# Optimization experiments

Measured on AMD Instinct MI355X. Metric: run time of the kernel, lower is better.

The kernel has to match this reference:

```python
import jax, jax.numpy as jnp
import numpy as np
import math

NUM_HEADS = 16  # power of two -> simple ALiBi slope formula

def alibi_slopes(num_heads: int) -> jnp.ndarray:
    # num_heads is a power of two here; general formula per Press et al. 2022
    k = 1 << (num_heads.bit_length() - 1)
    ratio = 2.0 ** (-8.0 / k)
    slopes = ratio ** np.arange(1, 1 + k)
    if num_heads != k:
        ratio2 = 2.0 ** (-8.0 / (2 * k))
        rest = (ratio2 ** np.arange(1, 1 + 2 * k, 2))[: num_heads - k]
        slopes = np.concatenate([slopes, rest])
    return jnp.asarray(slopes, dtype=jnp.float32).reshape(1, -1, 1, 1)


def setup_inputs() -> dict:
    key = jax.random.key(0)
    kq, kk, kv, km = jax.random.split(key, 4)
    B, H, S, D = 1, NUM_HEADS, 2048, 64
    query = jax.random.normal(kq, (B, H, S, D), dtype=jnp.float32)
    k_ = jax.random.normal(kk, (B, H, S, D), dtype=jnp.float32)
    value = jax.random.normal(kv, (B, H, S, D), dtype=jnp.float32)
    # padding-style boolean mask [B, S]; keep position 0 always valid
    mask = jax.random.randint(km, (B, S), 0, 2).astype(bool)
    mask = mask.at[:, 0].set(True)
    return {"query": query, "key": k_, "value": value, "mask": mask}


def reference(query, key, value, mask):
    B, H, S, D = query.shape
    scale = 1.0 / math.sqrt(D)
    # scores: [B, H, Sq, Sk]
    scores = jnp.einsum("bhqd,bhkd->bhqk", query, key) * scale
    # causal ALiBi bias: distances arange(1-S, 1) -> shape (1, H, 1, S)
    distances = jnp.arange(1 - S, 1, dtype=jnp.float32)
    bias = distances[None, None, None, :] * alibi_slopes(H)
    scores = scores + bias
    # boolean padding mask [B, S] -> [B, 1, 1, S]
    blocked = jnp.finfo(scores.dtype).min
    scores = jnp.where(mask[:, None, None, :], scores, blocked)
    weights = jax.nn.softmax(scores, axis=-1)
    # dropout_prob = 0.0 (eval) -> identity
    return jnp.einsum("bhqk,bhkd->bhqd", weights, value)
```

## Files before the change

kernel.cpp:

```cpp
#include <hip/hip_runtime.h>


constexpr int   S_LEN  = 2048;
constexpr int   D_DIM  = 64;
constexpr int   H_NUM  = 16;
constexpr int   QT     = 128;
constexpr int   K_TILE = 64;
constexpr int   NTILE  = S_LEN / K_TILE;
constexpr int   MAXNC  = 8;
constexpr int   QB     = S_LEN / QT;
constexpr int   PROWSTR= 36;
constexpr float SCL    = 0.18033688f;
constexpr float L2E    = 1.44269504f;
constexpr float MASKED = -50000.0f;
constexpr float CUTOFF = 40.0f;

typedef short bf16x8 __attribute__((ext_vector_type(8)));
typedef short bf16x4 __attribute__((ext_vector_type(4)));
typedef float f32x4  __attribute__((ext_vector_type(4)));

__device__ inline short f2bf(float f) {
    union { float f; unsigned u; } x; x.f = f;
    return (short)((x.u + 0x7fffu + ((x.u >> 16) & 1u)) >> 16);
}

__device__ inline unsigned pack2bf(float a, float b) {
#if __has_builtin(__builtin_amdgcn_cvt_pk_bf16_f32)
    auto p = __builtin_amdgcn_cvt_pk_bf16_f32(a, b);
    unsigned u; __builtin_memcpy(&u, &p, 4); return u;
#else
    return (unsigned)(unsigned short)f2bf(a) | ((unsigned)(unsigned short)f2bf(b) << 16);
#endif
}

__device__ inline float fexp2(float x) {
#if __has_builtin(__builtin_amdgcn_exp2f)
    return __builtin_amdgcn_exp2f(x);
#else
    return exp2f(x);
#endif
}

__device__ inline unsigned permb(unsigned hi, unsigned lo, unsigned sel) {
#if __has_builtin(__builtin_amdgcn_perm)
    return __builtin_amdgcn_perm(hi, lo, sel);
#else
    return (sel == 0x05040100u) ? ((lo & 0xffffu) | (hi << 16))
                                : ((lo >> 16) | (hi & 0xffff0000u));
#endif
}

__device__ inline void load_lds16(const void* g, void* l) {
    __builtin_amdgcn_global_load_lds((const __attribute__((address_space(1))) void*)g,
                                     (__attribute__((address_space(3))) void*)l, 16, 0, 0);
}

__device__ inline int head_t0(int h) {
    const float slope_l2e = exp2f(-0.5f * (float)(h + 1)) * L2E;
    const float kmin = 2047.0f - CUTOFF / slope_l2e;
    return kmin <= 0.0f ? 0 : ((int)kmin) >> 6;
}
__device__ inline int head_nc(int h) {
    const int nt = NTILE - head_t0(h);
    const int nc = (nt + 3) >> 2;
    return nc > MAXNC ? MAXNC : nc;
}

__global__ __launch_bounds__(256)
void preprocess_kernel(const float* __restrict__ Km, const float* __restrict__ Vm,
                       const void* __restrict__ maskp,
                       short* __restrict__ Kswz, short* __restrict__ Vswz,
                       float* __restrict__ Bias)
{
    __shared__ int mask_is_i32;
    const int tid = threadIdx.x;
    const int kt = blockIdx.x, h = blockIdx.y;
    if (kt < head_t0(h)) return;

    const int kbase = kt * K_TILE;
    const size_t tbase = ((size_t)h * S_LEN + kbase) * D_DIM;
    short* Kd = Kswz + ((size_t)h * NTILE + kt) * 4096;
    short* Vd = Vswz + ((size_t)h * NTILE + kt) * 4096;

    if (tid < 64) {
        const unsigned v = ((const unsigned*)maskp)[tid];
        const unsigned long long b = __ballot(v <= 1u);
        if (tid == 0) mask_is_i32 = (b == ~0ULL);
    }

    #pragma unroll
    for (int it = 0; it < 2; ++it) {
        const int idx = it * 256 + tid;
        const int key = idx >> 3, c = idx & 7;
        const float* src = Km + tbase + key * 64 + c * 8;
        float4 a = *(const float4*)src;
        float4 b = *(const float4*)(src + 4);
        unsigned u[4] = { pack2bf(a.x, a.y), pack2bf(a.z, a.w),
                          pack2bf(b.x, b.y), pack2bf(b.z, b.w) };
        bf16x8 kp; __builtin_memcpy(&kp, u, 16);
        *(bf16x8*)(Kd + key * 64 + ((c ^ (key & 7)) << 3)) = kp;
    }

    {
        const int db = tid >> 4, kb = tid & 15;
        const int d4 = db * 4, key4 = kb * 4;
        float4 vv[4];
        #pragma unroll
        for (int j = 0; j < 4; ++j)
            vv[j] = *(const float4*)(Vm + tbase + (key4 + j) * 64 + d4);
        const float* vp = (const float*)vv;
        #pragma unroll
        for (int jj = 0; jj < 4; ++jj) {
            const int d = d4 + jj;
            bf16x4 ov;
            ov[0] = f2bf(vp[0 * 4 + jj]); ov[1] = f2bf(vp[1 * 4 + jj]);
            ov[2] = f2bf(vp[2 * 4 + jj]); ov[3] = f2bf(vp[3 * 4 + jj]);
            *(bf16x4*)(Vd + d * 64 + (((key4 >> 3) ^ (d & 7)) << 3) + (key4 & 7)) = ov;
        }
    }
    __syncthreads();
    if (tid < K_TILE) {
        const int key = kbase + tid;
        const int mv = mask_is_i32 ? ((const int*)maskp)[key]
                                   : (int)((const unsigned char*)maskp)[key];
        const float slope_l2e = exp2f(-0.5f * (float)(h + 1)) * L2E;
        Bias[h * S_LEN + key] = mv ? slope_l2e * (float)(key - (S_LEN - 1)) : MASKED;
    }
}

__global__ __launch_bounds__(256, 4)
void attn_main(const float* __restrict__ Qm, const short* __restrict__ Kswz,
               const short* __restrict__ Vswz, const float* __restrict__ Bias,
               float* __restrict__ Om, float* __restrict__ Opart,
               float* __restrict__ lp)
{
    __shared__ short    k_lds[4096];
    __shared__ short    v_lds[4096];
    __shared__ float    bm_lds[64];
    __shared__ unsigned p_lds[4][32 * PROWSTR];

    const int tid = threadIdx.x;
    const int wave = tid >> 6, lane = tid & 63;
    const int l16 = lane & 15, quad = lane >> 4;
    const int h = blockIdx.y, qblk = blockIdx.x, c = blockIdx.z;

    const int nc = head_nc(h);
    if (c >= nc) return;
    const int t0 = head_t0(h);
    const int nt = NTILE - t0;
    const int tstart = t0 + (c * nt) / nc;
    const int tend   = t0 + ((c + 1) * nt) / nc;

    const unsigned psel = (quad < 2) ? 0x05040100u : 0x07060302u;

    bf16x8 qfrag[2][2];
    {
        const float* Qh = Qm + (size_t)h * S_LEN * D_DIM;
        #pragma unroll
        for (int s = 0; s < 2; ++s) {
            const int qrow = qblk * QT + wave * 32 + s * 16 + l16;
            #pragma unroll
            for (int t = 0; t < 2; ++t) {
                const float* src = Qh + (size_t)qrow * D_DIM + t * 32 + quad * 8;
                float4 a = *(const float4*)src;
                float4 b = *(const float4*)(src + 4);
                unsigned* qp = (unsigned*)&qfrag[s][t];
                qp[0] = pack2bf(a.x * SCL, a.y * SCL);
                qp[1] = pack2bf(a.z * SCL, a.w * SCL);
                qp[2] = pack2bf(b.x * SCL, b.y * SCL);
                qp[3] = pack2bf(b.z * SCL, b.w * SCL);
            }
        }
    }

    bf16x8 onesv;
    #pragma unroll
    for (int i = 0; i < 8; ++i) onesv[i] = (short)0x3F80;

    f32x4 o_frag[2][4], l4[2];
    #pragma unroll
    for (int s = 0; s < 2; ++s) {
        #pragma unroll
        for (int cc = 0; cc < 4; ++cc) o_frag[s][cc] = (f32x4){0.f, 0.f, 0.f, 0.f};
        l4[s] = (f32x4){0.f, 0.f, 0.f, 0.f};
    }

    const short* Kh = Kswz + (size_t)h * NTILE * 4096;
    const short* Vh = Vswz + (size_t)h * NTILE * 4096;
    const float* Bh = Bias + h * S_LEN;
    unsigned* pw = p_lds[wave];
    const int swz = l16 & 7;

    for (int kt = tstart; kt < tend; ++kt) {
        __syncthreads();
        {
            const char* kg = (const char*)(Kh + (size_t)kt * 4096);
            const char* vg = (const char*)(Vh + (size_t)kt * 4096);
            char* kl = (char*)k_lds + wave * 2048;
            char* vl = (char*)v_lds + wave * 2048;
            const int go = wave * 2048 + lane * 16;
            load_lds16(kg + go,        kl);
            load_lds16(kg + go + 1024, kl + 1024);
            load_lds16(vg + go,        vl);
            load_lds16(vg + go + 1024, vl + 1024);
        }
        if (tid < 16) {
            float4 b4 = *(const float4*)(Bh + kt * K_TILE + tid * 4);
            *(float4*)&bm_lds[tid * 4] = b4;
        }
        __syncthreads();

        f32x4 sv[2][4];
        #pragma unroll
        for (int cc = 0; cc < 4; ++cc) {
            const float b = bm_lds[cc * 16 + l16];
            const f32x4 binit = (f32x4){b, b, b, b};
            sv[0][cc] = binit;
            sv[1][cc] = binit;
            #pragma unroll
            for (int t = 0; t < 2; ++t) {
                bf16x8 bfrag = *(const bf16x8*)&k_lds[(cc * 16 + l16) * 64 + (((t * 4 + quad) ^ swz) << 3)];
                sv[0][cc] = __builtin_amdgcn_mfma_f32_16x16x32_bf16(qfrag[0][t], bfrag, sv[0][cc], 0, 0, 0);
                sv[1][cc] = __builtin_amdgcn_mfma_f32_16x16x32_bf16(qfrag[1][t], bfrag, sv[1][cc], 0, 0, 0);
            }
        }

        #pragma unroll
        for (int s = 0; s < 2; ++s) {
            #pragma unroll
            for (int r = 0; r < 4; ++r) {
                const float p0 = fexp2(sv[s][0][r]);
                const float p1 = fexp2(sv[s][1][r]);
                const float p2 = fexp2(sv[s][2][r]);
                const float p3 = fexp2(sv[s][3][r]);
                unsigned* pp = &pw[(s * 16 + quad * 4 + r) * PROWSTR + l16];
                pp[0]  = pack2bf(p0, p1);
                pp[16] = pack2bf(p2, p3);
            }
        }

        #pragma unroll
        for (int t2 = 0; t2 < 2; ++t2) {
            bf16x8 pfrag[2];
            #pragma unroll
            for (int s = 0; s < 2; ++s) {
                const unsigned* pr = &pw[(s * 16 + l16) * PROWSTR + t2 * 16 + (quad & 1) * 8];
                uint4 w0 = *(const uint4*)(pr);
                uint4 w1 = *(const uint4*)(pr + 4);
                unsigned pf[4];
                pf[0] = permb(w0.y, w0.x, psel);
                pf[1] = permb(w0.w, w0.z, psel);
                pf[2] = permb(w1.y, w1.x, psel);
                pf[3] = permb(w1.w, w1.z, psel);
                __builtin_memcpy(&pfrag[s], pf, 16);
            }
            #pragma unroll
            for (int c2 = 0; c2 < 4; ++c2) {
                bf16x8 vfrag = *(const bf16x8*)&v_lds[(c2 * 16 + l16) * 64 + (((t2 * 4 + quad) ^ swz) << 3)];
                o_frag[0][c2] = __builtin_amdgcn_mfma_f32_16x16x32_bf16(pfrag[0], vfrag, o_frag[0][c2], 0, 0, 0);
                o_frag[1][c2] = __builtin_amdgcn_mfma_f32_16x16x32_bf16(pfrag[1], vfrag, o_frag[1][c2], 0, 0, 0);
            }
            l4[0] = __builtin_amdgcn_mfma_f32_16x16x32_bf16(pfrag[0], onesv, l4[0], 0, 0, 0);
            l4[1] = __builtin_amdgcn_mfma_f32_16x16x32_bf16(pfrag[1], onesv, l4[1], 0, 0, 0);
        }
    }

    if (nc == 1) {
        float* Oh = Om + (size_t)h * S_LEN * D_DIM;
        const int qrow0 = qblk * QT + wave * 32;
        #pragma unroll
        for (int s = 0; s < 2; ++s) {
            #pragma unroll
            for (int r = 0; r < 4; ++r) {
                const float inv = 1.0f / l4[s][r];
                const int row = qrow0 + s * 16 + quad * 4 + r;
                float* dst = Oh + (size_t)row * D_DIM + l16;
                dst[0]  = o_frag[s][0][r] * inv;
                dst[16] = o_frag[s][1][r] * inv;
                dst[32] = o_frag[s][2][r] * inv;
                dst[48] = o_frag[s][3][r] * inv;
            }
        }
    } else {
        #pragma unroll
        for (int s = 0; s < 2; ++s) {
            const int g = qblk * 32 + wave * 8 + s * 4 + quad;
            const size_t gbase = (((size_t)h * MAXNC + c) * 512 + g);
            #pragma unroll
            for (int c2 = 0; c2 < 4; ++c2) {
                float* dst = Opart + (gbase * 64 + c2 * 16 + l16) * 4;
                *(f32x4*)dst = o_frag[s][c2];
            }
            if (l16 == 0) *(f32x4*)(lp + gbase * 4) = l4[s];
        }
    }
}

__global__ __launch_bounds__(256)
void attn_combine_kernel(const float* __restrict__ Opart, const float* __restrict__ lp,
                         float* __restrict__ Om)
{
    const int t   = blockIdx.x * 256 + threadIdx.x;
    const int col = t & 63;
    const int g   = (t >> 6) & 511;
    const int h   = t >> 15;

    const int nc = head_nc(h);
    if (nc == 1) return;

    f32x4 acc = (f32x4){0.f, 0.f, 0.f, 0.f};
    f32x4 den = (f32x4){0.f, 0.f, 0.f, 0.f};
    for (int c = 0; c < nc; ++c) {
        const size_t gbase = (((size_t)h * MAXNC + c) * 512 + g);
        den += *(const f32x4*)(lp + gbase * 4);
        acc += *(const f32x4*)(Opart + (gbase * 64 + col) * 4);
    }
    float* Oh = Om + (size_t)h * S_LEN * D_DIM;
    #pragma unroll
    for (int r = 0; r < 4; ++r)
        Oh[(size_t)(g * 4 + r) * 64 + col] = acc[r] / den[r];
}

extern "C" void kernel_launch(void* const* d_in, const int* in_sizes, int n_in,
                              void* d_out, int out_size, void* d_ws, size_t ws_size,
                              hipStream_t stream) {
    (void)in_sizes; (void)n_in; (void)out_size; (void)ws_size;
    const float* Q = (const float*)d_in[0];
    const float* K = (const float*)d_in[1];
    const float* V = (const float*)d_in[2];
    const void*  M = d_in[3];
    float* O = (float*)d_out;

    char* ws = (char*)d_ws;
    size_t off = 0;
    short* Kswz = (short*)(ws + off); off += (size_t)H_NUM * S_LEN * D_DIM * 2;
    short* Vswz = (short*)(ws + off); off += (size_t)H_NUM * S_LEN * D_DIM * 2;
    float* Bias = (float*)(ws + off); off += (size_t)H_NUM * S_LEN * 4;
    float* Opart = (float*)(ws + off); off += (size_t)H_NUM * MAXNC * 512 * 64 * 4 * 4;
    float* lp   = (float*)(ws + off); off += (size_t)H_NUM * MAXNC * 512 * 4 * 4;

    preprocess_kernel<<<dim3(NTILE, H_NUM), 256, 0, stream>>>(K, V, M, Kswz, Vswz, Bias);
    attn_main<<<dim3(QB, H_NUM, MAXNC), 256, 0, stream>>>(Q, Kswz, Vswz, Bias, O, Opart, lp);
    attn_combine_kernel<<<(H_NUM * 512 * 64) / 256, 256, 0, stream>>>(Opart, lp, O);
}
```

Baseline: 97.89 us.

## Fuse split-K combine into main kernel via atomic counter; bf16 partials and Q precast

Removes the separate combine kernel. The last-arriving split block for each (head, q-block), detected with an atomic counter, reduces the partial outputs and writes the final result. Partial outputs are now stored as bf16 instead of fp32, halving that traffic but adding rounding error. Q is converted to scaled bf16 in the preprocess kernel so the main kernel loads bf16 fragments directly. The trade-offs are precision loss in the partials, a fence/atomic sync tail in the main kernel, and extra preprocess work.

Measured after the change: 211.8 us. 116% more time.

```diff
diff --git a/kernel.cpp b/kernel.cpp
--- a/kernel.cpp
+++ b/kernel.cpp
@@ -67,14 +67,34 @@
 }
 
 __global__ __launch_bounds__(256)
-void preprocess_kernel(const float* __restrict__ Km, const float* __restrict__ Vm,
-                       const void* __restrict__ maskp,
-                       short* __restrict__ Kswz, short* __restrict__ Vswz,
-                       float* __restrict__ Bias)
+void preprocess_kernel(const float* __restrict__ Qm, const float* __restrict__ Km,
+                       const float* __restrict__ Vm, const void* __restrict__ maskp,
+                       short* __restrict__ Qbf, short* __restrict__ Kswz,
+                       short* __restrict__ Vswz, float* __restrict__ Bias,
+                       int* __restrict__ cnt)
 {
     __shared__ int mask_is_i32;
     const int tid = threadIdx.x;
     const int kt = blockIdx.x, h = blockIdx.y;
+
+    if (kt == 0 && tid < QB) cnt[h * QB + tid] = 0;
+
+    {
+        const int row = kt * 64 + (tid >> 2);
+        const int col = (tid & 3) << 4;
+        const float* src = Qm + ((size_t)h * S_LEN + row) * D_DIM + col;
+        short* dst = Qbf + ((size_t)h * S_LEN + row) * D_DIM + col;
+        #pragma unroll
+        for (int j = 0; j < 2; ++j) {
+            float4 a = *(const float4*)(src + j * 8);
+            float4 b = *(const float4*)(src + j * 8 + 4);
+            unsigned u[4] = { pack2bf(a.x * SCL, a.y * SCL), pack2bf(a.z * SCL, a.w * SCL),
+                              pack2bf(b.x * SCL, b.y * SCL), pack2bf(b.z * SCL, b.w * SCL) };
+            bf16x8 qp; __builtin_memcpy(&qp, u, 16);
+            *(bf16x8*)(dst + j * 8) = qp;
+        }
+    }
+
     if (kt < head_t0(h)) return;
 
     const int kbase = kt * K_TILE;
@@ -129,15 +149,16 @@
 }
 
 __global__ __launch_bounds__(256, 4)
-void attn_main(const float* __restrict__ Qm, const short* __restrict__ Kswz,
+void attn_main(const short* __restrict__ Qbf, const short* __restrict__ Kswz,
                const short* __restrict__ Vswz, const float* __restrict__ Bias,
-               float* __restrict__ Om, float* __restrict__ Opart,
-               float* __restrict__ lp)
+               float* __restrict__ Om, unsigned* __restrict__ Opart,
+               float* __restrict__ lp, int* __restrict__ cnt)
 {
     __shared__ short    k_lds[4096];
     __shared__ short    v_lds[4096];
     __shared__ float    bm_lds[64];
     __shared__ unsigned p_lds[4][32 * PROWSTR];
+    __shared__ int      arrive_old;
 
     const int tid = threadIdx.x;
     const int wave = tid >> 6, lane = tid & 63;
@@ -155,21 +176,13 @@
 
     bf16x8 qfrag[2][2];
     {
-        const float* Qh = Qm + (size_t)h * S_LEN * D_DIM;
+        const short* Qh = Qbf + (size_t)h * S_LEN * D_DIM;
         #pragma unroll
         for (int s = 0; s < 2; ++s) {
             const int qrow = qblk * QT + wave * 32 + s * 16 + l16;
             #pragma unroll
-            for (int t = 0; t < 2; ++t) {
-                const float* src = Qh + (size_t)qrow * D_DIM + t * 32 + quad * 8;
-                float4 a = *(const float4*)src;
-                float4 b = *(const float4*)(src + 4);
-                unsigned* qp = (unsigned*)&qfrag[s][t];
-                qp[0] = pack2bf(a.x * SCL, a.y * SCL);
-                qp[1] = pack2bf(a.z * SCL, a.w * SCL);
-                qp[2] = pack2bf(b.x * SCL, b.y * SCL);
-                qp[3] = pack2bf(b.z * SCL, b.w * SCL);
-            }
+            for (int t = 0; t < 2; ++t)
+                qfrag[s][t] = *(const bf16x8*)(Qh + (size_t)qrow * D_DIM + t * 32 + quad * 8);
         }
     }
 
@@ -281,44 +294,65 @@
                 dst[48] = o_frag[s][3][r] * inv;
             }
         }
-    } else {
-        #pragma unroll
-        for (int s = 0; s < 2; ++s) {
-            const int g = qblk * 32 + wave * 8 + s * 4 + quad;
-            const size_t gbase = (((size_t)h * MAXNC + c) * 512 + g);
-            #pragma unroll
-            for (int c2 = 0; c2 < 4; ++c2) {
-                float* dst = Opart + (gbase * 64 + c2 * 16 + l16) * 4;
-                *(f32x4*)dst = o_frag[s][c2];
-            }
-            if (l16 == 0) *(f32x4*)(lp + gbase * 4) = l4[s];
-        }
-    }
-}
-
-__global__ __launch_bounds__(256)
-void attn_combine_kernel(const float* __restrict__ Opart, const float* __restrict__ lp,
-                         float* __restrict__ Om)
-{
-    const int t   = blockIdx.x * 256 + threadIdx.x;
-    const int col = t & 63;
-    const int g   = (t >> 6) & 511;
-    const int h   = t >> 15;
-
-    const int nc = head_nc(h);
-    if (nc == 1) return;
-
-    f32x4 acc = (f32x4){0.f, 0.f, 0.f, 0.f};
-    f32x4 den = (f32x4){0.f, 0.f, 0.f, 0.f};
-    for (int c = 0; c < nc; ++c) {
+        return;
+    }
+
+    #pragma unroll
+    for (int s = 0; s < 2; ++s) {
+        const int g = qblk * 32 + wave * 8 + s * 4 + quad;
         const size_t gbase = (((size_t)h * MAXNC + c) * 512 + g);
-        den += *(const f32x4*)(lp + gbase * 4);
-        acc += *(const f32x4*)(Opart + (gbase * 64 + col) * 4);
-    }
-    float* Oh = Om + (size_t)h * S_LEN * D_DIM;
-    #pragma unroll
-    for (int r = 0; r < 4; ++r)
-        Oh[(size_t)(g * 4 + r) * 64 + col] = acc[r] / den[r];
+        #pragma unroll
+        for (int c2 = 0; c2 < 4; ++c2) {
+            uint2 pk;
+            pk.x = pack2bf(o_frag[s][c2][0], o_frag[s][c2][1]);
+            pk.y = pack2bf(o_frag[s][c2][2], o_frag[s][c2][3]);
+            *(uint2*)(Opart + (gbase * 64 + c2 * 16 + l16) * 2) = pk;
+        }
+        if (l16 == 0) *(f32x4*)(lp + gbase * 4) = l4[s];
+    }
+
+    __threadfence();
+    __syncthreads();
+    if (tid == 0) arrive_old = atomicAdd(&cnt[h * QB + qblk], 1);
+    __syncthreads();
+    if (arrive_old != nc - 1) return;
+    __threadfence();
+
+    {
+        const int gl = tid >> 3;
+        const int cb = (tid & 7) * 8;
+        const int g  = qblk * 32 + gl;
+
+        f32x4 den = (f32x4){0.f, 0.f, 0.f, 0.f};
+        for (int k = 0; k < nc; ++k)
+            den += *(const f32x4*)(lp + (((size_t)h * MAXNC + k) * 512 + g) * 4);
+        f32x4 inv;
+        #pragma unroll
+        for (int r = 0; r < 4; ++r) inv[r] = 1.0f / den[r];
+
+        float outv[4][8];
+        #pragma unroll
+        for (int j = 0; j < 8; ++j) {
+            f32x4 acc = (f32x4){0.f, 0.f, 0.f, 0.f};
+            for (int k = 0; k < nc; ++k) {
+                const size_t gbase = ((size_t)h * MAXNC + k) * 512 + g;
+                const uint2 pk = *(const uint2*)(Opart + (gbase * 64 + cb + j) * 2);
+                acc[0] += __int_as_float(pk.x << 16);
+                acc[1] += __int_as_float((int)(pk.x & 0xffff0000u));
+                acc[2] += __int_as_float(pk.y << 16);
+                acc[3] += __int_as_float((int)(pk.y & 0xffff0000u));
+            }
+            #pragma unroll
+            for (int r = 0; r < 4; ++r) outv[r][j] = acc[r] * inv[r];
+        }
+        float* Oh = Om + (size_t)h * S_LEN * D_DIM;
+        #pragma unroll
+        for (int r = 0; r < 4; ++r) {
+            float* dst = Oh + (size_t)(g * 4 + r) * D_DIM + cb;
+            *(float4*)dst = (float4){outv[r][0], outv[r][1], outv[r][2], outv[r][3]};
+            *(float4*)(dst + 4) = (float4){outv[r][4], outv[r][5], outv[r][6], outv[r][7]};
+        }
+    }
 }
 
 extern "C" void kernel_launch(void* const* d_in, const int* in_sizes, int n_in,
@@ -335,11 +369,12 @@
     size_t off = 0;
     short* Kswz = (short*)(ws + off); off += (size_t)H_NUM * S_LEN * D_DIM * 2;
     short* Vswz = (short*)(ws + off); off += (size_t)H_NUM * S_LEN * D_DIM * 2;
+    short* Qbf  = (short*)(ws + off); off += (size_t)H_NUM * S_LEN * D_DIM * 2;
     float* Bias = (float*)(ws + off); off += (size_t)H_NUM * S_LEN * 4;
-    float* Opart = (float*)(ws + off); off += (size_t)H_NUM * MAXNC * 512 * 64 * 4 * 4;
+    unsigned* Opart = (unsigned*)(ws + off); off += (size_t)H_NUM * MAXNC * 512 * 64 * 8;
     float* lp   = (float*)(ws + off); off += (size_t)H_NUM * MAXNC * 512 * 4 * 4;
-
-    preprocess_kernel<<<dim3(NTILE, H_NUM), 256, 0, stream>>>(K, V, M, Kswz, Vswz, Bias);
-    attn_main<<<dim3(QB, H_NUM, MAXNC), 256, 0, stream>>>(Q, Kswz, Vswz, Bias, O, Opart, lp);
-    attn_combine_kernel<<<(H_NUM * 512 * 64) / 256, 256, 0, stream>>>(Opart, lp, O);
-}
+    int*   cnt  = (int*)(ws + off);   off += (size_t)H_NUM * QB * 4;
+
+    preprocess_kernel<<<dim3(NTILE, H_NUM), 256, 0, stream>>>(Q, K, V, M, Qbf, Kswz, Vswz, Bias, cnt);
+    attn_main<<<dim3(QB, H_NUM, MAXNC), 256, 0, stream>>>(Qbf, Kswz, Vswz, Bias, O, Opart, lp, cnt);
+}
```
